# Performance work log

Hardware: AMD Instinct MI355X
Metric: run time of the kernel (lower is better)

## Reference

```python
import jax, jax.numpy as jnp
import numpy as np

# Standard NF4 quantization codebook (bitsandbytes values)
_NF4_CB = np.array([
    -1.0, -0.6961928009986877, -0.5250730514526367, -0.39491748809814453,
    -0.28444138169288635, -0.18477343022823334, -0.09105003625154495, 0.0,
    0.07958029955625534, 0.16093020141124725, 0.24611230194568634, 0.33791524171829224,
    0.44070982933044434, 0.5626170039176941, 0.7229568362236023, 1.0], dtype=np.float32)

B, L, H, E, DFF = 2, 2048, 2048, 8, 8192
BLK = 512  # NF4 quantization block size (b_idx = h // 512 in kernel)


def setup_inputs() -> dict:
    key = jax.random.key(0)
    ks = jax.random.split(key, 8)
    N = B * L
    x = jax.random.normal(ks[0], (B, L, H), dtype=jnp.float32)
    router_w = jax.random.normal(ks[1], (H, E), dtype=jnp.float32) * 0.02
    # packed NF4: one byte = two 4-bit codebook indices (low nibble -> even h)
    nf4 = jax.random.randint(ks[2], (N, E, H // 2), 0, 256, dtype=jnp.int32)
    mean = jax.random.normal(ks[3], (N, E, H // BLK), dtype=jnp.float32) * 0.01
    std = jax.random.uniform(ks[4], (N, E, H // BLK), dtype=jnp.float32) + 0.5
    codebook = jnp.asarray(_NF4_CB)
    w1 = jax.random.normal(ks[5], (H, DFF), dtype=jnp.float32) * 0.02
    w2 = jax.random.normal(ks[6], (DFF, H), dtype=jnp.float32) * 0.02
    return {"x": x, "router_w": router_w, "nf4": nf4, "mean": mean,
            "std": std, "codebook": codebook, "w1": w1, "w2": w2}


def reference(x, router_w, nf4, mean, std, codebook, w1, w2):
    b, l, h = x.shape
    n = b * l
    e = router_w.shape[1]
    xf = x.reshape(n, h)

    # shared expert MLP (base_mlp): Linear -> GELU -> Linear
    mlp = jax.nn.gelu(xf @ w1) @ w2  # [N, H]

    # router: logits in fp32, softmax, cast to fp16 as the kernel does
    logits = xf @ router_w  # [N, E]
    probs = jax.nn.softmax(logits, axis=-1).astype(jnp.float16).astype(jnp.float32)

    # NF4 unpack: low nibble -> even h, high nibble -> odd h
    low = nf4 & 15
    high = (nf4 >> 4) & 15
    idx = jnp.stack([low, high], axis=-1).reshape(n, e, h)  # interleave -> [N,E,H]
    vals = codebook[idx]  # codebook gather, [N,E,H]

    # per-block (512) rescale: val*std + mean
    nb = mean.shape[-1]
    blk = h // nb
    dq = (vals.reshape(n, e, nb, blk) * std[..., None] + mean[..., None]).reshape(n, e, h)

    # weighted expert mix + MLP residual add
    moe = jnp.einsum('ne,neh->nh', probs, dq)
    return (moe + mlp).reshape(b, l, h)
```

## Files before the change

kernel.cpp:

```cpp
#include <hip/hip_runtime.h>
#include <hip/hip_bf16.h>
#include <hip/hip_fp16.h>

#define H 2048
#define E 8
#define DFF 8192
#define NTOK 4096
#define NB 4

typedef _Float16 f16x8 __attribute__((ext_vector_type(8)));
typedef float f32x4 __attribute__((ext_vector_type(4)));

#define AS1 __attribute__((address_space(1)))
#define AS3 __attribute__((address_space(3)))

__device__ __forceinline__ void gl_lds16(const void* g, void* l) {
    __builtin_amdgcn_global_load_lds((const AS1 unsigned int*)g,
                                     (AS3 unsigned int*)l, 16, 0, 0);
}

__device__ __forceinline__ float gelu_f(float x) {
    float u = 0.7978845608028654f * x * (1.0f + 0.044715f * x * x);
    float t = fabsf(u);
    float e = __expf(-2.0f * t);
    float th = (1.0f - e) / (1.0f + e);
    th = copysignf(th, u);
    return 0.5f * x * (1.0f + th);
}

__global__ __launch_bounds__(256) void router_cast_kernel(
    const float* __restrict__ x, const float* __restrict__ rw,
    float* __restrict__ probs, _Float16* __restrict__ xh)
{
    int n = blockIdx.x, t = threadIdx.x;
    float acc[E];
#pragma unroll
    for (int e = 0; e < E; ++e) acc[e] = 0.f;
    const float* xr = x + (size_t)n * H;
#pragma unroll
    for (int k = 0; k < H / 256; ++k) {
        int h = t + k * 256;
        float xv = xr[h];
        xh[(size_t)n * H + h] = (_Float16)xv;
        const float4* r4 = reinterpret_cast<const float4*>(rw + (size_t)h * E);
        float4 a = r4[0], b = r4[1];
        acc[0] += xv * a.x; acc[1] += xv * a.y; acc[2] += xv * a.z; acc[3] += xv * a.w;
        acc[4] += xv * b.x; acc[5] += xv * b.y; acc[6] += xv * b.z; acc[7] += xv * b.w;
    }
#pragma unroll
    for (int e = 0; e < E; ++e) {
        float v = acc[e];
#pragma unroll
        for (int o = 32; o > 0; o >>= 1) v += __shfl_down(v, o, 64);
        acc[e] = v;
    }
    __shared__ float red[4][E];
    int wave = t >> 6, lane = t & 63;
    if (lane == 0) {
#pragma unroll
        for (int e = 0; e < E; ++e) red[wave][e] = acc[e];
    }
    __syncthreads();
    if (t == 0) {
        float lg[E];
        float mx = -1e30f;
#pragma unroll
        for (int e = 0; e < E; ++e) {
            lg[e] = red[0][e] + red[1][e] + red[2][e] + red[3][e];
            mx = fmaxf(mx, lg[e]);
        }
        float s = 0.f;
#pragma unroll
        for (int e = 0; e < E; ++e) { lg[e] = expf(lg[e] - mx); s += lg[e]; }
        float inv = 1.f / s;
#pragma unroll
        for (int e = 0; e < E; ++e) {
            float p = lg[e] * inv;
            p = __half2float(__float2half(p));
            probs[(size_t)n * E + e] = p;
        }
    }
}

__global__ __launch_bounds__(256) void transpose_cast_kernel(
    const float* __restrict__ src, _Float16* __restrict__ dst, int R, int C)
{
    __shared__ float tile[32][33];
    int tx = threadIdx.x & 31, ty = threadIdx.x >> 5;
    int c0 = blockIdx.x * 32, r0 = blockIdx.y * 32;
#pragma unroll
    for (int i = ty; i < 32; i += 8)
        tile[i][tx] = src[(size_t)(r0 + i) * C + c0 + tx];
    __syncthreads();
#pragma unroll
    for (int i = ty; i < 32; i += 8)
        dst[(size_t)(c0 + i) * R + r0 + tx] = (_Float16)tile[tx][i];
}

__global__ __launch_bounds__(256) void moe_kernel(
    const int* __restrict__ nf4, const float* __restrict__ mean,
    const float* __restrict__ stdv, const float* __restrict__ cb,
    const float* __restrict__ probs, float* __restrict__ moe)
{
    int n = blockIdx.x, t = threadIdx.x;
    __shared__ float cbl[32];
    __shared__ float ps[E][NB];
    __shared__ float cmean[NB];
    if (t < 16) { float v = cb[t]; cbl[t] = v; cbl[t + 16] = v; }
    else if (t >= 32 && t < 64) {
        int e = (t - 32) >> 2, b = t & 3;
        ps[e][b] = probs[(size_t)n * E + e] * stdv[((size_t)n * E + e) * NB + b];
    } else if (t >= 64 && t < 68) {
        int b = t - 64; float s = 0.f;
        for (int e = 0; e < E; ++e)
            s += probs[(size_t)n * E + e] * mean[((size_t)n * E + e) * NB + b];
        cmean[b] = s;
    }
    __syncthreads();
    int cboff = (t & 1) << 4;
    const int* w = nf4 + (size_t)n * (E * H / 2);
    float2* outp = reinterpret_cast<float2*>(moe + (size_t)n * H);
#pragma unroll
    for (int k = 0; k < 4; ++k) {
        int j = t + k * 256;
        float psr[E];
#pragma unroll
        for (int e = 0; e < E; ++e) psr[e] = ps[e][k];
        float cm = cmean[k];
        float aL = cm, aH = cm;
#pragma unroll
        for (int e = 0; e < E; ++e) {
            int word = w[e * (H / 2) + j];
            aL += psr[e] * cbl[(word & 15) + cboff];
            aH += psr[e] * cbl[((word >> 4) & 15) + cboff];
        }
        outp[j] = make_float2(aL, aH);
    }
}

template <int EPI, int MAP>
__global__ __launch_bounds__(512, 2) void gemm8p_kernel(
    const _Float16* __restrict__ A, const _Float16* __restrict__ Bt,
    const float* __restrict__ addsrc, void* __restrict__ outv,
    float* __restrict__ aux, int K, int LDK, int N)
{
    __shared__ uint4 lds_u4[131072 / 16];
    char* lds = (char*)lds_u4;
    char* R0 = lds;
    char* R1 = lds + 65536;

    int t = threadIdx.x;
    int id = blockIdx.x;
    int xcd = id & 7, chunk = id >> 3;
    int by, bx, ks = 0;
    if constexpr (MAP == 0) {
        by = (xcd & 1) * 8 + (chunk & 7);
        bx = (xcd >> 1) * 8 + (chunk >> 3);
    } else {
        by = (xcd >> 1) * 4 + (chunk & 3);
        bx = (xcd & 1) * 4 + ((chunk >> 2) & 3);
        ks = chunk >> 4;
    }
    int m0 = by * 256, n0 = bx * 256;
    int koff = ks * K;

    const unsigned short* sA = (const unsigned short*)A
        + (size_t)(m0 + (t & 255)) * LDK + koff + (t >> 8) * 8;
    const unsigned short* sB = (const unsigned short*)Bt
        + (size_t)(n0 + (t & 255)) * LDK + koff + (t >> 8) * 8;
    unsigned dstT = (unsigned)t * 16;

    int lane = t & 63, wave = t >> 6;
    int wr = wave >> 2, wc = wave & 3;
    int mb = wr * 128, nb = wc * 64;
    int q = lane >> 4, m16 = lane & 15;

    unsigned aBase = (unsigned)(mb + m16) * 16u;
    unsigned bBase = 32768u + (unsigned)(nb + m16) * 16u;

    f32x4 acc[8][4] = {};
    f16x8 af[8], bL[4], bH[4];

#define STG_A(Wb, T, s) do { \
    gl_lds16(sA + (size_t)(T) * 64 + (s) * 16,      (Wb) + (s) * 8192 + dstT); \
    gl_lds16(sA + (size_t)(T) * 64 + (s) * 16 + 16, (Wb) + (s) * 8192 + 8192 + dstT); } while (0)
#define STG_B(Wb, T, s) do { \
    gl_lds16(sB + (size_t)(T) * 64 + (s) * 16,      (Wb) + 32768 + (s) * 8192 + dstT); \
    gl_lds16(sB + (size_t)(T) * 64 + (s) * 16 + 16, (Wb) + 32768 + (s) * 8192 + 8192 + dstT); } while (0)
#define RD_A(Rb, ih) do { \
    _Pragma("unroll") for (int il = 0; il < 4; ++il) \
    _Pragma("unroll") for (int kh = 0; kh < 2; ++kh) \
        af[il * 2 + kh] = *(const f16x8*)((Rb) + aBase + \
            (unsigned)(kh * 16384 + q * 4096 + (ih) * 1024 + il * 256)); } while (0)
#define RD_B(Rb, jh, dst) do { \
    _Pragma("unroll") for (int jl = 0; jl < 2; ++jl) \
    _Pragma("unroll") for (int kh = 0; kh < 2; ++kh) \
        dst[jl * 2 + kh] = *(const f16x8*)((Rb) + bBase + \
            (unsigned)(kh * 16384 + q * 4096 + (jh) * 512 + jl * 256)); } while (0)
#define MMQ(ih, bfr, j0) do { \
    __builtin_amdgcn_s_setprio(1); \
    _Pragma("unroll") for (int il = 0; il < 4; ++il) \
    _Pragma("unroll") for (int jl = 0; jl < 2; ++jl) \
    _Pragma("unroll") for (int kh = 0; kh < 2; ++kh) \
        acc[(ih) * 4 + il][(j0) + jl] = __builtin_amdgcn_mfma_f32_16x16x32_f16( \
            af[il * 2 + kh], bfr[jl * 2 + kh], acc[(ih) * 4 + il][(j0) + jl], 0, 0, 0); \
    __builtin_amdgcn_s_setprio(0); } while (0)
#define BARR  asm volatile("s_barrier" ::: "memory")
#define LGKM0 asm volatile("s_waitcnt lgkmcnt(0)" ::: "memory")

    STG_A(R0, 0, 0); STG_A(R0, 0, 2);
    STG_B(R0, 0, 0); STG_B(R0, 0, 2);
    STG_A(R1, 1, 0);
    asm volatile("s_waitcnt vmcnt(2)" ::: "memory");
    BARR;

    int NIT = K / 128;
    for (int i = 0; i < NIT; ++i) {
        int T0 = 2 * i, T1 = 2 * i + 1;
        bool more = (i + 1 < NIT);

        STG_A(R1, T1, 2);
        RD_A(R0, 0); RD_B(R0, 0, bL);
        BARR; LGKM0;
        MMQ(0, bL, 0);
        BARR;
        STG_B(R1, T1, 0);
        RD_B(R0, 1, bH);
        BARR; LGKM0;
        MMQ(0, bH, 2);
        BARR;
        STG_B(R1, T1, 2);
        RD_A(R0, 1);
        BARR; LGKM0;
        MMQ(1, bH, 2);
        BARR;
        if (more) STG_A(R0, T0 + 2, 0);
        MMQ(1, bL, 0);
        if (more) asm volatile("s_waitcnt vmcnt(2)" ::: "memory");
        else      asm volatile("s_waitcnt vmcnt(0)" ::: "memory");
        BARR;

        if (more) STG_A(R0, T0 + 2, 2);
        RD_A(R1, 0); RD_B(R1, 0, bL);
        BARR; LGKM0;
        MMQ(0, bL, 0);
        BARR;
        if (more) STG_B(R0, T0 + 2, 0);
        RD_B(R1, 1, bH);
        BARR; LGKM0;
        MMQ(0, bH, 2);
        BARR;
        if (more) STG_B(R0, T0 + 2, 2);
        RD_A(R1, 1);
        BARR; LGKM0;
        MMQ(1, bH, 2);
        BARR;
        if (more) STG_A(R1, T1 + 2, 0);
        MMQ(1, bL, 0);
        if (more) asm volatile("s_waitcnt vmcnt(2)" ::: "memory");
        else      asm volatile("s_waitcnt vmcnt(0)" ::: "memory");
        BARR;
    }

#pragma unroll
    for (int i = 0; i < 8; ++i)
#pragma unroll
        for (int j = 0; j < 4; ++j) {
            int row = m0 + mb + i * 16 + q * 4;
            int col = n0 + nb + j * 16 + m16;
#pragma unroll
            for (int rix = 0; rix < 4; ++rix) {
                float v = acc[i][j][rix];
                size_t o = (size_t)(row + rix) * N + col;
                if constexpr (EPI == 0) {
                    ((_Float16*)outv)[o] = (_Float16)gelu_f(v);
                } else {
                    if (ks == 0) ((float*)outv)[o] = v + addsrc[o];
                    else         aux[o] = v;
                }
            }
        }
#undef STG_A
#undef STG_B
#undef RD_A
#undef RD_B
#undef MMQ
#undef BARR
#undef LGKM0
}

__global__ __launch_bounds__(256) void combine_kernel(
    float* __restrict__ out, const float* __restrict__ part)
{
    size_t base = (size_t)blockIdx.x * 256 + threadIdx.x;
    const float4* p4 = (const float4*)part;
    float4* o4 = (float4*)out;
#pragma unroll
    for (int s = 0; s < 4; ++s) {
        size_t i = base + (size_t)s * 524288;
        float4 a = o4[i], b = p4[i];
        o4[i] = make_float4(a.x + b.x, a.y + b.y, a.z + b.z, a.w + b.w);
    }
}

extern "C" void kernel_launch(void* const* d_in, const int* in_sizes, int n_in,
                              void* d_out, int out_size, void* d_ws, size_t ws_size,
                              hipStream_t stream) {
    const float* x    = (const float*)d_in[0];
    const float* rw   = (const float*)d_in[1];
    const int*   nf4  = (const int*)d_in[2];
    const float* mean = (const float*)d_in[3];
    const float* stdv = (const float*)d_in[4];
    const float* cb   = (const float*)d_in[5];
    const float* w1   = (const float*)d_in[6];
    const float* w2   = (const float*)d_in[7];
    float* out = (float*)d_out;

    char* ws = (char*)d_ws;
    float* probs      = (float*)ws;
    float* moe        = (float*)(ws + 131072);
    _Float16* xh      = (_Float16*)(ws + 33685504);
    _Float16* w1t     = (_Float16*)(ws + 50462720);
    _Float16* w2t     = (_Float16*)(ws + 84017152);
    _Float16* hid     = (_Float16*)(ws + 117571584);
    float* pbuf       = (float*)(ws + 50462720);

    router_cast_kernel<<<NTOK, 256, 0, stream>>>(x, rw, probs, xh);
    transpose_cast_kernel<<<dim3(DFF / 32, H / 32), 256, 0, stream>>>(w1, w1t, H, DFF);
    transpose_cast_kernel<<<dim3(H / 32, DFF / 32), 256, 0, stream>>>(w2, w2t, DFF, H);
    moe_kernel<<<NTOK, 256, 0, stream>>>(nf4, mean, stdv, cb, probs, moe);
    gemm8p_kernel<0, 0><<<512, 512, 0, stream>>>(xh, w1t, nullptr, (void*)hid,
                                                 nullptr, H, H, DFF);
    gemm8p_kernel<1, 1><<<256, 512, 0, stream>>>(hid, w2t, moe, (void*)out,
                                                 pbuf, DFF / 2, DFF, H);
    combine_kernel<<<2048, 256, 0, stream>>>(out, pbuf);
}
```

Before: 790.6 us.

## Restructure GEMM main loop with double-buffered register fragments and fewer barriers

Reworks the software pipeline of the 256x256 MFMA GEMM loop. A and B fragments are now double-buffered in registers (low and high halves), so LDS reads for the next sub-step are issued while MFMAs on the current fragments run. sched_barrier calls pin this interleaving, and the loop now uses two barriers per half-iteration instead of eight. Global-to-LDS staging is batched into four loads per operand with vmcnt(4) waits. The extra fragment registers raise VGPR pressure, and the buffer-reuse ordering must stay correct with fewer barriers.

```diff
diff --git a/kernel.cpp b/kernel.cpp
--- a/kernel.cpp
+++ b/kernel.cpp
@@ -179,87 +179,82 @@
     unsigned bBase = 32768u + (unsigned)(nb + m16) * 16u;
 
     f32x4 acc[8][4] = {};
-    f16x8 af[8], bL[4], bH[4];
-
-#define STG_A(Wb, T, s) do { \
-    gl_lds16(sA + (size_t)(T) * 64 + (s) * 16,      (Wb) + (s) * 8192 + dstT); \
-    gl_lds16(sA + (size_t)(T) * 64 + (s) * 16 + 16, (Wb) + (s) * 8192 + 8192 + dstT); } while (0)
-#define STG_B(Wb, T, s) do { \
-    gl_lds16(sB + (size_t)(T) * 64 + (s) * 16,      (Wb) + 32768 + (s) * 8192 + dstT); \
-    gl_lds16(sB + (size_t)(T) * 64 + (s) * 16 + 16, (Wb) + 32768 + (s) * 8192 + 8192 + dstT); } while (0)
-#define RD_A(Rb, ih) do { \
+    f16x8 aLf[8], aHf[8], blf[4], bhf[4];
+
+#define STG_A4(Wb, T) do { \
+    _Pragma("unroll") for (int s = 0; s < 4; ++s) \
+        gl_lds16(sA + (size_t)(T) * 64 + s * 16, (Wb) + s * 8192 + dstT); } while (0)
+#define STG_B4(Wb, T) do { \
+    _Pragma("unroll") for (int s = 0; s < 4; ++s) \
+        gl_lds16(sB + (size_t)(T) * 64 + s * 16, (Wb) + 32768 + s * 8192 + dstT); } while (0)
+#define RD_A(Rb, ih, dst) do { \
     _Pragma("unroll") for (int il = 0; il < 4; ++il) \
     _Pragma("unroll") for (int kh = 0; kh < 2; ++kh) \
-        af[il * 2 + kh] = *(const f16x8*)((Rb) + aBase + \
+        dst[il * 2 + kh] = *(const f16x8*)((Rb) + aBase + \
             (unsigned)(kh * 16384 + q * 4096 + (ih) * 1024 + il * 256)); } while (0)
 #define RD_B(Rb, jh, dst) do { \
     _Pragma("unroll") for (int jl = 0; jl < 2; ++jl) \
     _Pragma("unroll") for (int kh = 0; kh < 2; ++kh) \
         dst[jl * 2 + kh] = *(const f16x8*)((Rb) + bBase + \
             (unsigned)(kh * 16384 + q * 4096 + (jh) * 512 + jl * 256)); } while (0)
-#define MMQ(ih, bfr, j0) do { \
-    __builtin_amdgcn_s_setprio(1); \
+#define MM(i0, j0, afr, bfr) do { \
     _Pragma("unroll") for (int il = 0; il < 4; ++il) \
     _Pragma("unroll") for (int jl = 0; jl < 2; ++jl) \
     _Pragma("unroll") for (int kh = 0; kh < 2; ++kh) \
-        acc[(ih) * 4 + il][(j0) + jl] = __builtin_amdgcn_mfma_f32_16x16x32_f16( \
-            af[il * 2 + kh], bfr[jl * 2 + kh], acc[(ih) * 4 + il][(j0) + jl], 0, 0, 0); \
-    __builtin_amdgcn_s_setprio(0); } while (0)
+        acc[(i0) + il][(j0) + jl] = __builtin_amdgcn_mfma_f32_16x16x32_f16( \
+            afr[il * 2 + kh], bfr[jl * 2 + kh], acc[(i0) + il][(j0) + jl], 0, 0, 0); } while (0)
 #define BARR  asm volatile("s_barrier" ::: "memory")
 #define LGKM0 asm volatile("s_waitcnt lgkmcnt(0)" ::: "memory")
-
-    STG_A(R0, 0, 0); STG_A(R0, 0, 2);
-    STG_B(R0, 0, 0); STG_B(R0, 0, 2);
-    STG_A(R1, 1, 0);
-    asm volatile("s_waitcnt vmcnt(2)" ::: "memory");
+#define VMC4  asm volatile("s_waitcnt vmcnt(4)" ::: "memory")
+#define VMC0  asm volatile("s_waitcnt vmcnt(0)" ::: "memory")
+#define SCB   __builtin_amdgcn_sched_barrier(0)
+#define SP1   __builtin_amdgcn_s_setprio(1)
+#define SP0   __builtin_amdgcn_s_setprio(0)
+
+    STG_A4(R0, 0);
+    STG_B4(R0, 0);
+    STG_A4(R1, 1);
+    VMC4;
     BARR;
+    RD_A(R0, 0, aLf);
+    RD_B(R0, 0, blf);
+    RD_B(R0, 1, bhf);
 
     int NIT = K / 128;
     for (int i = 0; i < NIT; ++i) {
-        int T0 = 2 * i, T1 = 2 * i + 1;
+        int tt = 2 * i, u = tt + 1;
         bool more = (i + 1 < NIT);
 
-        STG_A(R1, T1, 2);
-        RD_A(R0, 0); RD_B(R0, 0, bL);
-        BARR; LGKM0;
-        MMQ(0, bL, 0);
+        STG_B4(R1, u);
+        RD_A(R0, 1, aHf);
+        SCB;
+        SP1; MM(0, 2, aLf, bhf); SCB; MM(0, 0, aLf, blf); SP0;
+        LGKM0;
         BARR;
-        STG_B(R1, T1, 0);
-        RD_B(R0, 1, bH);
-        BARR; LGKM0;
-        MMQ(0, bH, 2);
+        if (more) STG_A4(R0, tt + 2);
+        if (more) { VMC4; } else { VMC0; }
         BARR;
-        STG_B(R1, T1, 2);
-        RD_A(R0, 1);
-        BARR; LGKM0;
-        MMQ(1, bH, 2);
+        SCB;
+        RD_A(R1, 0, aLf);
+        SCB; SP1; MM(4, 2, aHf, bhf); SCB;
+        RD_B(R1, 1, bhf);
+        SCB; MM(4, 0, aHf, blf); SP0; SCB;
+        RD_B(R1, 0, blf);
+        if (more) STG_B4(R0, tt + 2);
+        RD_A(R1, 1, aHf);
+        SCB;
+        SP1; MM(0, 2, aLf, bhf); SCB; MM(0, 0, aLf, blf); SP0;
+        LGKM0;
         BARR;
-        if (more) STG_A(R0, T0 + 2, 0);
-        MMQ(1, bL, 0);
-        if (more) asm volatile("s_waitcnt vmcnt(2)" ::: "memory");
-        else      asm volatile("s_waitcnt vmcnt(0)" ::: "memory");
+        if (more) STG_A4(R1, tt + 3);
+        if (more) { VMC4; } else { VMC0; }
         BARR;
-
-        if (more) STG_A(R0, T0 + 2, 2);
-        RD_A(R1, 0); RD_B(R1, 0, bL);
-        BARR; LGKM0;
-        MMQ(0, bL, 0);
-        BARR;
-        if (more) STG_B(R0, T0 + 2, 0);
-        RD_B(R1, 1, bH);
-        BARR; LGKM0;
-        MMQ(0, bH, 2);
-        BARR;
-        if (more) STG_B(R0, T0 + 2, 2);
-        RD_A(R1, 1);
-        BARR; LGKM0;
-        MMQ(1, bH, 2);
-        BARR;
-        if (more) STG_A(R1, T1 + 2, 0);
-        MMQ(1, bL, 0);
-        if (more) asm volatile("s_waitcnt vmcnt(2)" ::: "memory");
-        else      asm volatile("s_waitcnt vmcnt(0)" ::: "memory");
-        BARR;
+        SCB;
+        if (more) RD_A(R0, 0, aLf);
+        SCB; SP1; MM(4, 2, aHf, bhf); SCB;
+        if (more) RD_B(R0, 1, bhf);
+        SCB; MM(4, 0, aHf, blf); SP0; SCB;
+        if (more) RD_B(R0, 0, blf);
     }
 
 #pragma unroll
@@ -280,13 +275,18 @@
                 }
             }
         }
-#undef STG_A
-#undef STG_B
+#undef STG_A4
+#undef STG_B4
 #undef RD_A
 #undef RD_B
-#undef MMQ
+#undef MM
 #undef BARR
 #undef LGKM0
+#undef VMC4
+#undef VMC0
+#undef SCB
+#undef SP1
+#undef SP0
 }
 
 __global__ __launch_bounds__(256) void combine_kernel(
```

Result: no change. 792.2 us (+0.2%).
